# Kernel tuning notes

Hardware: AMD Instinct MI355X
Metric: run time of the kernel (lower is better)

Reference implementation:

```python
import jax, jax.numpy as jnp
import numpy as np

N, C, H, W = 8, 256, 128, 128
HD = 256          # hidden_depth
FC, FS, CS = 8, 2, 8  # heads_count, fold_size, center_size
EPS_GN = 1e-5


def setup_inputs() -> dict:
    key = jax.random.key(0)
    ks = jax.random.split(key, 8)
    d = {
        'x': jax.random.normal(ks[0], (N, C, H, W), jnp.float32),
        'proj_w': jax.random.normal(ks[1], (2 * HD, C), jnp.float32) * 0.02,
        'proj_b': jnp.zeros((2 * HD,), jnp.float32),
        'merge_w': jax.random.normal(ks[2], (C, HD), jnp.float32) * 0.02,
        'merge_b': jnp.zeros((C,), jnp.float32),
        'alpha': jnp.ones((1,), jnp.float32),
        'beta': jnp.zeros((1,), jnp.float32),
        'g0_w': jnp.ones((C,), jnp.float32),
        'g0_b': jnp.zeros((C,), jnp.float32),
        'mlp_w0': jax.random.normal(ks[3], (2 * C, 2 * C), jnp.float32) * 0.02,
        'mlp_b0': jnp.zeros((2 * C,), jnp.float32),
        'mlp_w1': jax.random.normal(ks[4], (2 * C, C), jnp.float32) * 0.02,
        'mlp_b1': jnp.zeros((C,), jnp.float32),
        'g1_w': jnp.ones((C,), jnp.float32),
        'g1_b': jnp.zeros((C,), jnp.float32),
        'layer_scale': jnp.full((C,), 1e-5, jnp.float32),
    }
    return d


def _group_norm1(x, w, b):
    # GroupNorm(1, C): normalize over (C,H,W) per sample, per-channel affine
    mu = x.mean(axis=(1, 2, 3), keepdims=True)
    var = ((x - mu) ** 2).mean(axis=(1, 2, 3), keepdims=True)
    xn = (x - mu) * jax.lax.rsqrt(var + EPS_GN)
    return xn * w[None, :, None, None] + b[None, :, None, None]


def _l2norm(v):
    return v / jnp.maximum(jnp.linalg.norm(v, axis=-1, keepdims=True), 1e-12)


def _local_cluster(x, proj_w, proj_b, merge_w, merge_b, alpha, beta):
    n = x.shape[0]
    # 1x1 conv proj: C -> 2*HD
    y = jnp.einsum('nchw,oc->nohw', x, proj_w) + proj_b[None, :, None, None]
    c = y.shape[1] // FC              # per-head channels (2*HD/FC)
    h, w = H // FS, W // FS
    # 'n (fc c) (fh h) (fw w) -> (n fc fh fw) c h w'
    y = y.reshape(n, FC, c, FS, h, FS, w).transpose(0, 1, 3, 5, 2, 4, 6)
    y = y.reshape(n * FC * FS * FS, c, h, w)
    m = y.shape[0]
    # adaptive avg pool to CSxCS (h,w divisible by CS -> uniform pooling)
    center = y.reshape(m, c, CS, h // CS, CS, w // CS).mean(axis=(3, 5))
    L, s = h * w, CS * CS
    yf = y.reshape(m, c, L).transpose(0, 2, 1)       # [m, L, c]
    cf = center.reshape(m, c, s).transpose(0, 2, 1)  # [m, s, c]
    cv = c // 2
    x_point, x_value = yf[..., :cv], yf[..., cv:]
    c_point, c_value = cf[..., :cv], cf[..., cv:]
    sim = jnp.einsum('mlc,msc->mls', _l2norm(x_point), _l2norm(c_point))
    sim = jax.nn.sigmoid(alpha * sim + beta)         # [m, L, s]
    vals = sim.max(axis=2)                           # [m, L]
    idx = sim.argmax(axis=2) + s * jnp.arange(m)[:, None]
    vals = vals.reshape(-1)
    idx = idx.reshape(-1)
    xv = x_value.reshape(-1, cv)
    cvv = c_value.reshape(-1, cv)
    xv_aug = jnp.concatenate([xv, jnp.ones((xv.shape[0], 1), xv.dtype)], axis=1)
    cv_aug = jnp.concatenate([cvv, jnp.ones((cvv.shape[0], 1), cvv.dtype)], axis=1)
    # scatter-add weighted points into centers
    nc = cv_aug.at[idx].add(vals[:, None] * xv_aug)
    nc = nc[:, :-1] / nc[:, -1:]
    # gather back
    nx = vals[:, None] * nc[idx]                     # [m*L, cv]
    # '(n fc fh fw h w) c -> n (fc c) (fh h) (fw w)'
    nx = nx.reshape(n, FC, FS, FS, h, w, cv).transpose(0, 1, 6, 2, 4, 3, 5)
    nx = nx.reshape(n, FC * cv, H, W)                # [n, HD, H, W]
    return jnp.einsum('nchw,oc->nohw', nx, merge_w) + merge_b[None, :, None, None]


def reference(x, proj_w, proj_b, merge_w, merge_b, alpha, beta, g0_w, g0_b,
              mlp_w0, mlp_b0, mlp_w1, mlp_b1, g1_w, g1_b, layer_scale):
    new_x = _local_cluster(x, proj_w, proj_b, merge_w, merge_b, alpha, beta)
    new_x = _group_norm1(new_x, g0_w, g0_b)
    t = jnp.concatenate([x, new_x], axis=1)          # [n, 2C, H, W]
    t = t.transpose(0, 2, 3, 1)                      # NHWC
    t = jax.nn.gelu(t @ mlp_w0 + mlp_b0, approximate=False)
    t = t @ mlp_w1 + mlp_b1
    t = t.transpose(0, 3, 1, 2)                      # NCHW
    t = _group_norm1(t, g1_w, g1_b)
    t = t * layer_scale[None, :, None, None]
    return t + x
```

## Files before the change

### kernel.cpp

```cpp
#include <hip/hip_runtime.h>
#include <math.h>

#define PIX   16384
#define NB    8
#define CIN   256

typedef __attribute__((ext_vector_type(8))) short    short8;
typedef __attribute__((ext_vector_type(4))) float    f32x4;
typedef __attribute__((ext_vector_type(4))) unsigned short us4;
typedef __attribute__((ext_vector_type(8))) unsigned short us8;
typedef __attribute__((ext_vector_type(4))) unsigned char uc4;

__device__ __forceinline__ float bf2f(unsigned short h) {
  return __uint_as_float(((unsigned int)h) << 16);
}
__device__ __forceinline__ unsigned short f2bf(float f) {
  unsigned int u = __float_as_uint(f);
  return (unsigned short)((u + 0x7FFFu + ((u >> 16) & 1u)) >> 16);
}
__device__ __forceinline__ float gelu_f(float v) {
  return 0.5f * v * (1.f + erff(v * 0.70710678118654752f));
}

__device__ __forceinline__ unsigned fmono(float f) {
  const unsigned u = __float_as_uint(f);
  return (u & 0x80000000u) ? ~u : (u | 0x80000000u);
}

__device__ __forceinline__ unsigned umax16(unsigned v) {
  unsigned t;
  t = (unsigned)__builtin_amdgcn_update_dpp((int)v, (int)v, 0x121, 0xF, 0xF, false); v = v > t ? v : t;
  t = (unsigned)__builtin_amdgcn_update_dpp((int)v, (int)v, 0x122, 0xF, 0xF, false); v = v > t ? v : t;
  t = (unsigned)__builtin_amdgcn_update_dpp((int)v, (int)v, 0x124, 0xF, 0xF, false); v = v > t ? v : t;
  t = (unsigned)__builtin_amdgcn_update_dpp((int)v, (int)v, 0x128, 0xF, 0xF, false); v = v > t ? v : t;
  return v;
}
__device__ __forceinline__ int imin16(int v) {
  int t;
  t = __builtin_amdgcn_update_dpp(v, v, 0x121, 0xF, 0xF, false); v = v < t ? v : t;
  t = __builtin_amdgcn_update_dpp(v, v, 0x122, 0xF, 0xF, false); v = v < t ? v : t;
  t = __builtin_amdgcn_update_dpp(v, v, 0x124, 0xF, 0xF, false); v = v < t ? v : t;
  t = __builtin_amdgcn_update_dpp(v, v, 0x128, 0xF, 0xF, false); v = v < t ? v : t;
  return v;
}

__global__ void zero_kernel(float* p, int n) {
  int i = blockIdx.x * blockDim.x + threadIdx.x;
  if (i < n) p[i] = 0.f;
}

__global__ void prep_weights(const float* __restrict__ pw_f, const float* __restrict__ mw_f,
                             const float* __restrict__ w0, const float* __restrict__ w1,
                             unsigned short* __restrict__ pw, unsigned short* __restrict__ mw,
                             unsigned short* __restrict__ w0t, unsigned short* __restrict__ w1t,
                             unsigned short* __restrict__ pwF) {
  const int S1 = 512 * 256, S2 = 256 * 256, S3 = 512 * 512, S4 = 256 * 512, S5 = 512 * 256;
  int i = blockIdx.x * 256 + threadIdx.x;
  if (i < S1) { pw[i] = f2bf(pw_f[i]); return; }
  i -= S1;
  if (i < S2) { mw[i] = f2bf(mw_f[i]); return; }
  i -= S2;
  if (i < S3) { int o = i >> 9, k = i & 511; w0t[i] = f2bf(w0[k * 512 + o]); return; }
  i -= S3;
  if (i < S4) { int o = i >> 9, k = i & 511; w1t[i] = f2bf(w1[k * 256 + o]); return; }
  i -= S4;
  if (i < S5) {
    const int j = i & 7, lane = (i >> 3) & 63, ks = (i >> 9) & 7, ct = (i >> 12) & 3, f = i >> 14;
    const int ch = f * 64 + ct * 16 + (lane & 15);
    const int k  = ks * 32 + (lane >> 4) * 8 + j;
    pwF[i] = f2bf(pw_f[ch * 256 + k]);
  }
}

__global__ __launch_bounds__(256) void x_to_nhwc(const float* __restrict__ x,
                                                 unsigned short* __restrict__ xT) {
  __shared__ float tile[64][65];
  const int t = threadIdx.x;
  const int p0 = blockIdx.x * 64, c0 = blockIdx.y * 64, n = blockIdx.z;
#pragma unroll
  for (int i = 0; i < 4; i++) {
    const int c = i * 16 + (t >> 4);
    const float4 v = *(const float4*)(x + ((size_t)(n * 256 + c0 + c) << 14) + p0 + (t & 15) * 4);
    tile[c][(t & 15) * 4]     = v.x;
    tile[c][(t & 15) * 4 + 1] = v.y;
    tile[c][(t & 15) * 4 + 2] = v.z;
    tile[c][(t & 15) * 4 + 3] = v.w;
  }
  __syncthreads();
#pragma unroll
  for (int i = 0; i < 4; i++) {
    const int pp = i * 16 + (t >> 4);
    const int cl = (t & 15) * 4;
    us4 o;
    o.x = f2bf(tile[cl][pp]); o.y = f2bf(tile[cl + 1][pp]);
    o.z = f2bf(tile[cl + 2][pp]); o.w = f2bf(tile[cl + 3][pp]);
    *(us4*)&xT[(((size_t)n << 14) + p0 + pp) * 256 + c0 + cl] = o;
  }
}

template<bool CONCAT, bool GELU, bool STATS>
__global__ __launch_bounds__(256, 4) void mfma_gemm(
    const unsigned short* __restrict__ A, const float* __restrict__ bias,
    const unsigned short* __restrict__ B1, const unsigned short* __restrict__ B2,
    unsigned short* __restrict__ Y, int M, int K, int K1,
    int astride, int bstride, float* __restrict__ sums) {
  __shared__ unsigned short As[8192];
  __shared__ unsigned short Bs[8192];
  __shared__ float r1[4], r2[4];
  const int t = threadIdx.x;
  const int lane = t & 63, w = t >> 6;
  const int quad = lane >> 4, l16 = lane & 15;
  const int p0 = blockIdx.x * 128, m0 = blockIdx.y * 128;
  const int n = blockIdx.z;
  const int wm = w & 1, wn = w >> 1;
  const int K2 = K - K1;

  A += (size_t)n * astride;
  const size_t nb = ((size_t)n << 14);

  const unsigned short* gaP[4];
  const unsigned short* gb1P[4];
  const unsigned short* gb2P[4];
#pragma unroll
  for (int i = 0; i < 4; i++) {
    const int c = (w << 2) | i;
    const int tm = c >> 1, kk = c & 1;
    const int krow0 = kk * 32 + quad * 8;
    gaP[i] = A + (size_t)(m0 + tm * 16 + l16) * K + krow0;
    const int prow = p0 + tm * 16 + l16;
    gb1P[i] = B1 + (nb + prow) * (size_t)K1 + krow0;
    gb2P[i] = CONCAT ? (B2 + (nb + prow) * (size_t)K2 + krow0) : B1;
  }

  f32x4 acc[4][4];
#pragma unroll
  for (int im = 0; im < 4; im++)
#pragma unroll
    for (int in = 0; in < 4; in++) acc[im][in] = (f32x4)0.f;

  auto kstep = [&](bool second) {
    __syncthreads();
#pragma unroll
    for (int i = 0; i < 4; i++) {
      const int c = (w << 2) | i;
      __builtin_amdgcn_global_load_lds((const __attribute__((address_space(1))) void*)gaP[i],
          (__attribute__((address_space(3))) void*)&As[c * 512], 16, 0, 0);
      gaP[i] += 64;
      const unsigned short* gb = second ? gb2P[i] : gb1P[i];
      __builtin_amdgcn_global_load_lds((const __attribute__((address_space(1))) void*)gb,
          (__attribute__((address_space(3))) void*)&Bs[c * 512], 16, 0, 0);
      if (second) gb2P[i] += 64; else gb1P[i] += 64;
    }
    __syncthreads();
#pragma unroll
    for (int kk = 0; kk < 2; kk++) {
      short8 af[4], bfr[4];
#pragma unroll
      for (int im = 0; im < 4; im++)
        af[im] = *(const short8*)&As[(((wm * 4 + im) * 2 + kk) * 64 + lane) * 8];
#pragma unroll
      for (int in = 0; in < 4; in++)
        bfr[in] = *(const short8*)&Bs[(((wn * 4 + in) * 2 + kk) * 64 + lane) * 8];
#pragma unroll
      for (int im = 0; im < 4; im++)
#pragma unroll
        for (int in = 0; in < 4; in++)
          acc[im][in] = __builtin_amdgcn_mfma_f32_16x16x32_bf16(af[im], bfr[in], acc[im][in], 0, 0, 0);
    }
  };

  const int K1end = CONCAT ? K1 : K;
  for (int k0 = 0; k0 < K1end; k0 += 64) kstep(false);
  if (CONCAT) {
    for (int k0 = K1; k0 < K; k0 += 64) kstep(true);
  }

  float s = 0.f, s2 = 0.f;
#pragma unroll
  for (int im = 0; im < 4; im++) {
    const int om = m0 + (wm * 4 + im) * 16 + quad * 4;
    const f32x4 bv = *(const f32x4*)(bias + (size_t)n * bstride + om);
#pragma unroll
    for (int in = 0; in < 4; in++) {
      const int p = p0 + (wn * 4 + in) * 16 + l16;
      float v0 = acc[im][in].x + bv.x;
      float v1 = acc[im][in].y + bv.y;
      float v2 = acc[im][in].z + bv.z;
      float v3 = acc[im][in].w + bv.w;
      if (GELU) { v0 = gelu_f(v0); v1 = gelu_f(v1); v2 = gelu_f(v2); v3 = gelu_f(v3); }
      if (STATS) {
        s += (v0 + v1) + (v2 + v3);
        s2 = fmaf(v0, v0, s2); s2 = fmaf(v1, v1, s2);
        s2 = fmaf(v2, v2, s2); s2 = fmaf(v3, v3, s2);
      }
      us4 o4;
      o4.x = f2bf(v0); o4.y = f2bf(v1); o4.z = f2bf(v2); o4.w = f2bf(v3);
      *(us4*)&Y[(nb + p) * M + om] = o4;
    }
  }
  if (STATS) {
#pragma unroll
    for (int off = 32; off > 0; off >>= 1) {
      s += __shfl_down(s, off);
      s2 += __shfl_down(s2, off);
    }
    if (lane == 0) { r1[w] = s; r2[w] = s2; }
    __syncthreads();
    if (t == 0) {
      atomicAdd(&sums[2 * n],     (r1[0] + r1[1]) + (r1[2] + r1[3]));
      atomicAdd(&sums[2 * n + 1], (r2[0] + r2[1]) + (r2[2] + r2[3]));
    }
  }
}


__global__ __launch_bounds__(256) void xmeans_kernel(
    const unsigned short* __restrict__ xT, float* __restrict__ xmean) {
  const int reg = blockIdx.y, ksl = blockIdx.x;
  const int nn = reg >> 2, s1 = (reg >> 1) & 1, s2 = reg & 1;
  const int t = threadIdx.x;
  const int b = t >> 2, cg = t & 3;
  const int k0 = ksl * 32 + cg * 8;
  const size_t nbase = ((size_t)nn << 14);
  const int pr0 = s1 * 64 + (b >> 3) * 8, pc0 = s2 * 64 + (b & 7) * 8;
  float a8[8] = {0.f, 0.f, 0.f, 0.f, 0.f, 0.f, 0.f, 0.f};
#pragma unroll 1
  for (int r = 0; r < 8; r++) {
#pragma unroll
    for (int c = 0; c < 8; c++) {
      const us8 v = *(const us8*)(xT + (nbase + (size_t)(pr0 + r) * 128 + pc0 + c) * 256 + k0);
#pragma unroll
      for (int j = 0; j < 8; j++) a8[j] += bf2f(v[j]);
    }
  }
  float* o = xmean + (((size_t)(reg * 64 + b)) << 8) + k0;
  f32x4 o0, o1;
  o0.x = a8[0] * (1.f / 64.f); o0.y = a8[1] * (1.f / 64.f);
  o0.z = a8[2] * (1.f / 64.f); o0.w = a8[3] * (1.f / 64.f);
  o1.x = a8[4] * (1.f / 64.f); o1.y = a8[5] * (1.f / 64.f);
  o1.z = a8[6] * (1.f / 64.f); o1.w = a8[7] * (1.f / 64.f);
  *(f32x4*)o = o0;
  *(f32x4*)(o + 4) = o1;
}

__global__ __launch_bounds__(256) void centers_kernel(
    const float* __restrict__ xmean, const unsigned short* __restrict__ pw,
    const float* __restrict__ proj_bp, unsigned short* __restrict__ cpnh_g,
    float* __restrict__ cval_g) {
  const int m = blockIdx.x;
  const int nn = m >> 5, f = (m >> 2) & 7, s1 = (m >> 1) & 1, s2 = m & 1;
  const int reg = (nn << 2) | (s1 << 1) | s2;
  const int t = threadIdx.x;
  const int b = t >> 2, cg = t & 3;
  __shared__ float cs[64][68];

  {
    const float* xm = xmean + (((size_t)(reg * 64 + b)) << 8);
    float acc16[16];
#pragma unroll
    for (int c = 0; c < 16; c++) acc16[c] = 0.f;
#pragma unroll 1
    for (int k = 0; k < 256; k += 8) {
      float xv[8];
#pragma unroll
      for (int j = 0; j < 8; j++) xv[j] = xm[k + j];
#pragma unroll
      for (int c = 0; c < 16; c++) {
        const us8 wv = *(const us8*)(pw + (size_t)(f * 64 + cg * 16 + c) * 256 + k);
#pragma unroll
        for (int j = 0; j < 8; j++) acc16[c] = fmaf(bf2f(wv[j]), xv[j], acc16[c]);
      }
    }
#pragma unroll
    for (int c = 0; c < 16; c++)
      cs[b][cg * 16 + c] = acc16[c] + proj_bp[f * 64 + cg * 16 + c];
  }
  __syncthreads();

  {
    const int b2 = t >> 2, jg = t & 3;
    const f32x4 ov0 = *(const f32x4*)&cs[b2][32 + jg * 8];
    const f32x4 ov1 = *(const f32x4*)&cs[b2][32 + jg * 8 + 4];
    *(f32x4*)&cval_g[(((size_t)(m * 64 + b2)) << 5) + jg * 8]     = ov0;
    *(f32x4*)&cval_g[(((size_t)(m * 64 + b2)) << 5) + jg * 8 + 4] = ov1;
    float s = 0.f;
#pragma unroll
    for (int cc = 0; cc < 32; cc++) { const float v = cs[b2][cc]; s = fmaf(v, v, s); }
    const float inv = 1.f / fmaxf(sqrtf(s), 1e-12f);
    us4 o0, o1;
    o0.x = f2bf(cs[b2][jg * 8] * inv);     o0.y = f2bf(cs[b2][jg * 8 + 1] * inv);
    o0.z = f2bf(cs[b2][jg * 8 + 2] * inv); o0.w = f2bf(cs[b2][jg * 8 + 3] * inv);
    o1.x = f2bf(cs[b2][jg * 8 + 4] * inv); o1.y = f2bf(cs[b2][jg * 8 + 5] * inv);
    o1.z = f2bf(cs[b2][jg * 8 + 6] * inv); o1.w = f2bf(cs[b2][jg * 8 + 7] * inv);
    *(us4*)&cpnh_g[(((size_t)(m * 64 + b2)) << 5) + jg * 8]     = o0;
    *(us4*)&cpnh_g[(((size_t)(m * 64 + b2)) << 5) + jg * 8 + 4] = o1;
  }
}

__global__ __launch_bounds__(256, 3) void assign_kernel(
    const unsigned short* __restrict__ xT, const unsigned short* __restrict__ pwF,
    const float* __restrict__ proj_bp, const unsigned short* __restrict__ cpnh_g,
    const float* __restrict__ alpha_p, const float* __restrict__ beta_p,
    float* __restrict__ svals_g, unsigned char* __restrict__ sbest_g,
    float* __restrict__ accp_v, float* __restrict__ accp_c) {
  const int m = blockIdx.y, slice = blockIdx.x;
  const int n = m >> 5, f = (m >> 2) & 7, s1 = (m >> 1) & 1, s2 = m & 1;
  const int t = threadIdx.x;
  const int wave = t >> 6, lane = t & 63;
  const int quad = lane >> 4, l16 = lane & 15;
  const float alpha = alpha_p[0], beta = beta_p[0];

  __shared__ unsigned short ytile[16][2][64][8];
  __shared__ float svalss[256];
  __shared__ unsigned char sidxs[256];

  const size_t nbase = ((size_t)n << 14);
  const int prow0 = s1 * 64, pcol0 = s2 * 64;

  const short8 cb0 = *(const short8*)&cpnh_g[((size_t)(m * 64 +  0 + l16) << 5) + quad * 8];
  const short8 cb1 = *(const short8*)&cpnh_g[((size_t)(m * 64 + 16 + l16) << 5) + quad * 8];
  const short8 cb2 = *(const short8*)&cpnh_g[((size_t)(m * 64 + 32 + l16) << 5) + quad * 8];
  const short8 cb3 = *(const short8*)&cpnh_g[((size_t)(m * 64 + 48 + l16) << 5) + quad * 8];
  const int sl4 = (((l16 >> 2) << 4) | (l16 & 3)) << 2;

  float pb[4];
#pragma unroll
  for (int ct = 0; ct < 4; ct++) pb[ct] = proj_bp[f * 64 + ct * 16 + l16];

  {
    f32x4 acc[4][4];
#pragma unroll
    for (int pt = 0; pt < 4; pt++)
#pragma unroll
      for (int ct = 0; ct < 4; ct++) acc[pt][ct] = (f32x4)0.f;
    const unsigned short* xp[4];
#pragma unroll
    for (int pt = 0; pt < 4; pt++) {
      const int pidx = slice * 256 + wave * 64 + pt * 16;
      const int pix = (prow0 + (pidx >> 6)) * 128 + pcol0 + (pidx & 63) + l16;
      xp[pt] = xT + (nbase + pix) * (size_t)256 + quad * 8;
    }
    const unsigned short* pwb = pwF + ((size_t)f << 14) + lane * 8;
#pragma unroll 1
    for (int ks = 0; ks < 8; ks++) {
      short8 af[4], bf_[4];
#pragma unroll
      for (int pt = 0; pt < 4; pt++)
        af[pt] = *(const short8*)(xp[pt] + ks * 32);
#pragma unroll
      for (int ct = 0; ct < 4; ct++)
        bf_[ct] = *(const short8*)(pwb + (ct * 8 + ks) * 512);
#pragma unroll
      for (int pt = 0; pt < 4; pt++)
#pragma unroll
        for (int ct = 0; ct < 4; ct++)
          acc[pt][ct] = __builtin_amdgcn_mfma_f32_16x16x32_bf16(af[pt], bf_[ct], acc[pt][ct], 0, 0, 0);
    }
#pragma unroll
    for (int pt = 0; pt < 4; pt++) {
      const int tileG = wave * 4 + pt;
#pragma unroll
      for (int ct = 0; ct < 4; ct++) {
        const int ch = ct * 16 + l16;
        const int half = ch >> 5, chm = ch & 31;
        const int dq = chm >> 3, j = chm & 7;
#pragma unroll
        for (int r = 0; r < 4; r++) {
          const float v = acc[pt][ct][r] + pb[ct];
          ytile[tileG][half][dq * 16 + (quad * 4 + r)][j] = f2bf(v);
        }
      }
    }
  }
  __syncthreads();

#pragma unroll 1
  for (int tt = 0; tt < 4; tt++) {
    const int tile = wave * 4 + tt;
    const short8 apt = *(const short8*)&ytile[tile][0][quad * 16 + l16][0];

    float nrm = 0.f;
#pragma unroll
    for (int j = 0; j < 8; j++) {
      const float fv = bf2f((unsigned short)apt[j]);
      nrm = fmaf(fv, fv, nrm);
    }
    nrm += __shfl_xor(nrm, 16);
    nrm += __shfl_xor(nrm, 32);
    const float inva = 1.f / fmaxf(sqrtf(nrm), 1e-12f);

    const f32x4 d0 = __builtin_amdgcn_mfma_f32_16x16x32_bf16(apt, cb0, (f32x4)0.f, 0, 0, 0);
    const f32x4 d1 = __builtin_amdgcn_mfma_f32_16x16x32_bf16(apt, cb1, (f32x4)0.f, 0, 0, 0);
    const f32x4 d2 = __builtin_amdgcn_mfma_f32_16x16x32_bf16(apt, cb2, (f32x4)0.f, 0, 0, 0);
    const f32x4 d3 = __builtin_amdgcn_mfma_f32_16x16x32_bf16(apt, cb3, (f32x4)0.f, 0, 0, 0);

    float bv[4]; int bi[4];
#pragma unroll
    for (int r = 0; r < 4; r++) {
      const unsigned u0 = fmono(d0[r]);
      const unsigned u1 = fmono(d1[r]);
      const unsigned u2 = fmono(d2[r]);
      const unsigned u3 = fmono(d3[r]);
      unsigned mx = u0 > u1 ? u0 : u1;
      const unsigned mxb = u2 > u3 ? u2 : u3;
      mx = mx > mxb ? mx : mxb;
      mx = umax16(mx);
      int c0 = (u0 == mx) ? l16        : 64;
      int c1 = (u1 == mx) ? (16 + l16) : 64;
      int c2 = (u2 == mx) ? (32 + l16) : 64;
      int c3 = (u3 == mx) ? (48 + l16) : 64;
      int ci = c0 < c1 ? c0 : c1;
      const int cb = c2 < c3 ? c2 : c3;
      ci = ci < cb ? ci : cb;
      ci = imin16(ci);
      bi[r] = ci;
      bv[r] = __uint_as_float((mx & 0x80000000u) ? (mx ^ 0x80000000u) : ~mx);
    }

    const float rv01 = (l16 & 1) ? bv[1] : bv[0];
    const float rv23 = (l16 & 1) ? bv[3] : bv[2];
    const float rowv = (l16 & 2) ? rv23 : rv01;
    const int   ri01 = (l16 & 1) ? bi[1] : bi[0];
    const int   ri23 = (l16 & 1) ? bi[3] : bi[2];
    const int   rowi = (l16 & 2) ? ri23 : ri01;
    const unsigned pk = (__float_as_uint(rowv) & ~63u) | (unsigned)rowi;
    const unsigned got = (unsigned)__builtin_amdgcn_ds_bpermute(sl4, (int)pk);
    const int   idx = (int)(got & 63u);
    const float dot = __uint_as_float(got & ~63u);

    const float val = 1.f / (1.f + __expf(-fmaf(alpha, dot * inva, beta)));
    if (quad == 0) {
      const int pidxg = slice * 256 + tile * 16 + l16;
      svals_g[(size_t)m * 4096 + pidxg] = val;
      sbest_g[(size_t)m * 4096 + pidxg] = (unsigned char)idx;
      svalss[tile * 16 + l16] = val;
      sidxs[tile * 16 + l16] = (unsigned char)idx;
    }
  }
  __syncthreads();

  {
    const int b = t >> 2, g = t & 3;
    float a8[8] = {0.f, 0.f, 0.f, 0.f, 0.f, 0.f, 0.f, 0.f};
    float ac = 0.f;
#pragma unroll 4
    for (int p4 = 0; p4 < 64; p4++) {
      const uc4 i4 = *(const uc4*)&sidxs[p4 * 4];
#pragma unroll
      for (int u = 0; u < 4; u++) {
        const int idx = (u == 0) ? i4.x : (u == 1) ? i4.y : (u == 2) ? i4.z : i4.w;
        if (idx == b) {
          const int p = p4 * 4 + u;
          const float val = svalss[p];
          const us8 yv = *(const us8*)&ytile[p >> 4][1][(g << 4) | (p & 15)][0];
#pragma unroll
          for (int j = 0; j < 8; j++) a8[j] = fmaf(val, bf2f(yv[j]), a8[j]);
          ac += val;
        }
      }
    }
    const size_t pbx = ((size_t)(m * 16 + slice)) * 64;
    f32x4 o0, o1;
    o0.x = a8[0]; o0.y = a8[1]; o0.z = a8[2]; o0.w = a8[3];
    o1.x = a8[4]; o1.y = a8[5]; o1.z = a8[6]; o1.w = a8[7];
    *(f32x4*)&accp_v[(pbx + b) * 32 + g * 8]     = o0;
    *(f32x4*)&accp_v[(pbx + b) * 32 + g * 8 + 4] = o1;
    if (g == 0) accp_c[pbx + b] = ac;
  }
}

__global__ __launch_bounds__(256) void gather_kernel(
    const float* __restrict__ accp_v, const float* __restrict__ accp_c,
    const float* __restrict__ cval_g, const float* __restrict__ svals_g,
    const unsigned char* __restrict__ sbest_g, unsigned short* __restrict__ nx) {
  const int m = blockIdx.y, slice = blockIdx.x;
  const int n = m >> 5, f = (m >> 2) & 7, s1 = (m >> 1) & 1, s2 = m & 1;
  const int t = threadIdx.x;
  __shared__ float cm[64][34];

  const size_t nbase = ((size_t)n << 14);
  const int prow0 = s1 * 64, pcol0 = s2 * 64;

  for (int i = t; i < 2048; i += 256) {
    const int b = i >> 5, q = i & 31;
    float s = cval_g[((size_t)(m * 64 + b) << 5) + q];
    float c = 1.f;
#pragma unroll
    for (int s16 = 0; s16 < 16; s16++) {
      const size_t pbx = ((size_t)(m * 16 + s16)) * 64 + b;
      s += accp_v[pbx * 32 + q];
      c += accp_c[pbx];
    }
    cm[b][q] = s / c;
  }
  __syncthreads();

#pragma unroll
  for (int pass = 0; pass < 2; pass++) {
    const int l = slice * 512 + pass * 256 + t;
    const int p = (prow0 + (l >> 6)) * 128 + pcol0 + (l & 63);
    const float v = svals_g[(size_t)m * 4096 + l];
    const int b = sbest_g[(size_t)m * 4096 + l];
    unsigned short* nr = nx + (nbase + p) * 256 + f * 32;
#pragma unroll
    for (int q8 = 0; q8 < 4; q8++) {
      const float2 a0 = *(const float2*)&cm[b][q8 * 8];
      const float2 a1 = *(const float2*)&cm[b][q8 * 8 + 2];
      const float2 a2 = *(const float2*)&cm[b][q8 * 8 + 4];
      const float2 a3 = *(const float2*)&cm[b][q8 * 8 + 6];
      us8 o;
      o[0] = f2bf(v * a0.x); o[1] = f2bf(v * a0.y);
      o[2] = f2bf(v * a1.x); o[3] = f2bf(v * a1.y);
      o[4] = f2bf(v * a2.x); o[5] = f2bf(v * a2.y);
      o[6] = f2bf(v * a3.x); o[7] = f2bf(v * a3.y);
      *(us8*)&nr[q8 * 8] = o;
    }
  }
}

__global__ void gn_finalize0(const float* __restrict__ sums, const float* __restrict__ g0w,
                             const float* __restrict__ g0b, float* __restrict__ scl,
                             float* __restrict__ bia) {
  const int n = blockIdx.x, c = threadIdx.x;
  const float cntinv = 1.f / (float)(CIN * PIX);
  const float mu = sums[2 * n] * cntinv;
  const float var = sums[2 * n + 1] * cntinv - mu * mu;
  const float rs = rsqrtf(var + 1e-5f);
  const float a = rs * g0w[c];
  scl[n * 256 + c] = a;
  bia[n * 256 + c] = g0b[c] - mu * a;
}

__global__ void w0_scale(const unsigned short* __restrict__ w0t,
                         const float* __restrict__ scl, unsigned short* __restrict__ w0s) {
  const int n = blockIdx.y;
  const int i = blockIdx.x * 256 + threadIdx.x;
  const int k = i & 511;
  unsigned short v = w0t[i];
  if (k >= 256) v = f2bf(bf2f(v) * scl[n * 256 + k - 256]);
  w0s[(size_t)n * 262144 + i] = v;
}

__global__ void b0_eff(const unsigned short* __restrict__ w0t, const float* __restrict__ b0,
                       const float* __restrict__ bia, float* __restrict__ b0e) {
  const int n = blockIdx.y;
  const int o = blockIdx.x * 256 + threadIdx.x;
  float s = b0[o];
  const unsigned short* wr = w0t + (size_t)o * 512 + 256;
  const float* br = bia + n * 256;
#pragma unroll 4
  for (int k = 0; k < 256; k++) s = fmaf(bf2f(wr[k]), br[k], s);
  b0e[n * 512 + o] = s;
}

__global__ __launch_bounds__(256) void final_transpose(
    const unsigned short* __restrict__ u, const float* __restrict__ x,
    const float* __restrict__ sums, const float* __restrict__ g1w,
    const float* __restrict__ g1b, const float* __restrict__ lsc,
    float* __restrict__ out) {
  __shared__ float tile[64][68];
  const int t = threadIdx.x;
  const int p0 = blockIdx.x * 64, c0 = blockIdx.y * 64, n = blockIdx.z;
  {
    const int pl = t >> 2, g = t & 3;
    const unsigned short* up = u + ((((size_t)n << 14) + p0 + pl) << 8) + c0 + g * 16;
    const us8 v0 = *(const us8*)up;
    const us8 v1 = *(const us8*)(up + 8);
#pragma unroll
    for (int j = 0; j < 8; j++) {
      tile[pl][g * 16 + j] = bf2f(v0[j]);
      tile[pl][g * 16 + 8 + j] = bf2f(v1[j]);
    }
  }
  __syncthreads();
  {
    const int cl = t >> 2, g = t & 3;
    const int c = c0 + cl;
    const float cntinv = 1.f / (float)(CIN * PIX);
    const float mu = sums[2 * n] * cntinv;
    const float var = sums[2 * n + 1] * cntinv - mu * mu;
    const float rs = rsqrtf(var + 1e-5f);
    const float gw = rs * g1w[c] * lsc[c];
    const float gb = (g1b[c] - mu * rs * g1w[c]) * lsc[c];
    const size_t rowb = ((size_t)(n * 256 + c) << 14) + p0 + g * 16;
#pragma unroll
    for (int q = 0; q < 4; q++) {
      const float4 xv = *(const float4*)(x + rowb + q * 4);
      float4 o;
      o.x = fmaf(tile[g * 16 + q * 4][cl], gw, gb) + xv.x;
      o.y = fmaf(tile[g * 16 + q * 4 + 1][cl], gw, gb) + xv.y;
      o.z = fmaf(tile[g * 16 + q * 4 + 2][cl], gw, gb) + xv.z;
      o.w = fmaf(tile[g * 16 + q * 4 + 3][cl], gw, gb) + xv.w;
      *(float4*)(out + rowb + q * 4) = o;
    }
  }
}

extern "C" void kernel_launch(void* const* d_in, const int* in_sizes, int n_in,
                              void* d_out, int out_size, void* d_ws, size_t ws_size,
                              hipStream_t stream) {
  const float* x       = (const float*)d_in[0];
  const float* proj_w  = (const float*)d_in[1];
  const float* proj_b  = (const float*)d_in[2];
  const float* merge_w = (const float*)d_in[3];
  const float* merge_b = (const float*)d_in[4];
  const float* alpha   = (const float*)d_in[5];
  const float* beta    = (const float*)d_in[6];
  const float* g0w     = (const float*)d_in[7];
  const float* g0b     = (const float*)d_in[8];
  const float* w0      = (const float*)d_in[9];
  const float* b0      = (const float*)d_in[10];
  const float* w1      = (const float*)d_in[11];
  const float* b1      = (const float*)d_in[12];
  const float* g1w     = (const float*)d_in[13];
  const float* g1b     = (const float*)d_in[14];
  const float* lsc     = (const float*)d_in[15];
  float* out = (float*)d_out;

  unsigned short* wsu = (unsigned short*)d_ws;
  unsigned short* xT  = wsu;
  unsigned short* y   = xT + (size_t)33554432;
  unsigned short* nx  = y + (size_t)67108864;
  unsigned short* pw  = nx + (size_t)33554432;
  unsigned short* mw  = pw + 131072;
  unsigned short* w0t = mw + 65536;
  unsigned short* w1t = w0t + 262144;
  unsigned short* w0s = w1t + 131072;
  float* sums = (float*)(w0s + (size_t)2097152);
  float* scl0 = sums + 32;
  float* bia0 = scl0 + 2048;
  float* b0e  = bia0 + 2048;
  unsigned short* pwF = (unsigned short*)(b0e + 4096);
  float* xmean = (float*)y;
  unsigned short* newx = (unsigned short*)d_out;

  float* svals_g = (float*)((char*)d_out + 67108864);
  float* cval_g  = svals_g + 1048576;
  float* accp_v  = cval_g + 524288;
  float* accp_c  = accp_v + 8388608;
  unsigned short* cpnh_g = (unsigned short*)(accp_c + 262144);
  unsigned char*  sbest_g = (unsigned char*)(cpnh_g + 524288);

  zero_kernel<<<1, 64, 0, stream>>>(sums, 32);
  prep_weights<<<2816, 256, 0, stream>>>(proj_w, merge_w, w0, w1, pw, mw, w0t, w1t, pwF);
  x_to_nhwc<<<dim3(256, 4, NB), 256, 0, stream>>>(x, xT);

  xmeans_kernel<<<dim3(8, 32), 256, 0, stream>>>(xT, xmean);
  centers_kernel<<<256, 256, 0, stream>>>(xmean, pw, proj_b, cpnh_g, cval_g);
  assign_kernel<<<dim3(16, 256), 256, 0, stream>>>(
      xT, pwF, proj_b, cpnh_g, alpha, beta, svals_g, sbest_g, accp_v, accp_c);
  gather_kernel<<<dim3(8, 256), 256, 0, stream>>>(
      accp_v, accp_c, cval_g, svals_g, sbest_g, nx);

  mfma_gemm<false, false, true><<<dim3(128, 2, NB), 256, 0, stream>>>(
      mw, merge_b, nx, nullptr, newx, 256, 256, 256, 0, 0, sums);

  gn_finalize0<<<NB, 256, 0, stream>>>(sums, g0w, g0b, scl0, bia0);
  w0_scale<<<dim3(1024, NB), 256, 0, stream>>>(w0t, scl0, w0s);
  b0_eff<<<dim3(2, NB), 256, 0, stream>>>(w0t, b0, bia0, b0e);

  mfma_gemm<true, true, false><<<dim3(128, 4, NB), 256, 0, stream>>>(
      w0s, b0e, xT, newx, y, 512, 512, 256, 262144, 512, nullptr);

  mfma_gemm<false, false, true><<<dim3(128, 2, NB), 256, 0, stream>>>(
      w1t, b1, y, nullptr, nx, 256, 512, 512, 0, 0, sums + 16);

  final_transpose<<<dim3(256, 4, NB), 256, 0, stream>>>(
      nx, x, sums + 16, g1w, g1b, lsc, out);
}
```

Baseline: 942.2 us.

## Double-buffer B tiles in LDS and read weight fragments directly from global

```diff
diff --git a/kernel.cpp b/kernel.cpp
--- a/kernel.cpp
+++ b/kernel.cpp
@@ -104,8 +104,7 @@
     const unsigned short* __restrict__ B1, const unsigned short* __restrict__ B2,
     unsigned short* __restrict__ Y, int M, int K, int K1,
     int astride, int bstride, float* __restrict__ sums) {
-  __shared__ unsigned short As[8192];
-  __shared__ unsigned short Bs[8192];
+  __shared__ unsigned short Bs[2][8192];
   __shared__ float r1[4], r2[4];
   const int t = threadIdx.x;
   const int lane = t & 63, w = t >> 6;
@@ -118,7 +117,11 @@
   A += (size_t)n * astride;
   const size_t nb = ((size_t)n << 14);
 
-  const unsigned short* gaP[4];
+  const unsigned short* aP[4];
+#pragma unroll
+  for (int im = 0; im < 4; im++)
+    aP[im] = A + (size_t)(m0 + (wm * 4 + im) * 16 + l16) * K + quad * 8;
+
   const unsigned short* gb1P[4];
   const unsigned short* gb2P[4];
 #pragma unroll
@@ -126,7 +129,6 @@
     const int c = (w << 2) | i;
     const int tm = c >> 1, kk = c & 1;
     const int krow0 = kk * 32 + quad * 8;
-    gaP[i] = A + (size_t)(m0 + tm * 16 + l16) * K + krow0;
     const int prow = p0 + tm * 16 + l16;
     gb1P[i] = B1 + (nb + prow) * (size_t)K1 + krow0;
     gb2P[i] = CONCAT ? (B2 + (nb + prow) * (size_t)K2 + krow0) : B1;
@@ -138,41 +140,49 @@
 #pragma unroll
     for (int in = 0; in < 4; in++) acc[im][in] = (f32x4)0.f;
 
-  auto kstep = [&](bool second) {
-    __syncthreads();
+  const int ns  = K >> 6;
+  const int ns1 = (CONCAT ? K1 : K) >> 6;
+
+  auto stageB = [&](int bi, bool second) {
 #pragma unroll
     for (int i = 0; i < 4; i++) {
       const int c = (w << 2) | i;
-      __builtin_amdgcn_global_load_lds((const __attribute__((address_space(1))) void*)gaP[i],
-          (__attribute__((address_space(3))) void*)&As[c * 512], 16, 0, 0);
-      gaP[i] += 64;
       const unsigned short* gb = second ? gb2P[i] : gb1P[i];
       __builtin_amdgcn_global_load_lds((const __attribute__((address_space(1))) void*)gb,
-          (__attribute__((address_space(3))) void*)&Bs[c * 512], 16, 0, 0);
+          (__attribute__((address_space(3))) void*)&Bs[bi][c * 512], 16, 0, 0);
       if (second) gb2P[i] += 64; else gb1P[i] += 64;
     }
-    __syncthreads();
+  };
+
+  stageB(0, CONCAT && (0 >= ns1));
+  for (int s = 0; s < ns; s++) {
+    if (s + 1 < ns) {
+      stageB((s + 1) & 1, CONCAT && ((s + 1) >= ns1));
+      asm volatile("s_waitcnt vmcnt(4)" ::: "memory");
+    } else {
+      asm volatile("s_waitcnt vmcnt(0)" ::: "memory");
+    }
+    __builtin_amdgcn_sched_barrier(0);
+    __builtin_amdgcn_s_barrier();
+    const unsigned short* bbase = &Bs[s & 1][0];
 #pragma unroll
     for (int kk = 0; kk < 2; kk++) {
       short8 af[4], bfr[4];
 #pragma unroll
       for (int im = 0; im < 4; im++)
-        af[im] = *(const short8*)&As[(((wm * 4 + im) * 2 + kk) * 64 + lane) * 8];
+        af[im] = *(const short8*)(aP[im] + kk * 32);
 #pragma unroll
       for (int in = 0; in < 4; in++)
-        bfr[in] = *(const short8*)&Bs[(((wn * 4 + in) * 2 + kk) * 64 + lane) * 8];
+        bfr[in] = *(const short8*)&bbase[(((wn * 4 + in) * 2 + kk) * 64 + lane) * 8];
 #pragma unroll
       for (int im = 0; im < 4; im++)
 #pragma unroll
         for (int in = 0; in < 4; in++)
           acc[im][in] = __builtin_amdgcn_mfma_f32_16x16x32_bf16(af[im], bfr[in], acc[im][in], 0, 0, 0);
     }
-  };
-
-  const int K1end = CONCAT ? K1 : K;
-  for (int k0 = 0; k0 < K1end; k0 += 64) kstep(false);
-  if (CONCAT) {
-    for (int k0 = K1; k0 < K; k0 += 64) kstep(true);
+#pragma unroll
+    for (int im = 0; im < 4; im++) aP[im] += 64;
+    __builtin_amdgcn_s_barrier();
   }
 
   float s = 0.f, s2 = 0.f;
```

Result: slower. 1.071 ms (+13.7%).
